# Performance work log

Hardware: AMD Instinct MI355X
Metric: run time of the kernel (lower is better)

Reference implementation:

```python
import jax, jax.numpy as jnp
import numpy as np

# ---- static ragged-batch / paging layout (known at trace time) ----
B = 4
Q_LENS = np.array([256, 512, 128, 384])        # new tokens per sequence
HIST = np.array([1792, 1024, 1536, 768])       # cached history per sequence
KV_LENS = Q_LENS + HIST
BS = 64                                        # paged-cache block size
NUM_BLOCKS = 128
H, D = 32, 128
HID = H * D
TOTAL_Q = int(Q_LENS.sum())                    # 1280 packed tokens
MAX_Q = int(Q_LENS.max())
MAX_KV = int(KV_LENS.max())
NBLK = (KV_LENS + BS - 1) // BS
MAX_BLOCKS = int(NBLK.max())                   # 32
ROPE_BASE = 10000.0

Q_START = np.concatenate([[0], np.cumsum(Q_LENS)[:-1]])
TOK_SEQ = np.repeat(np.arange(B), Q_LENS)                      # [TOTAL_Q]
TOK_LOCAL = np.concatenate([np.arange(l) for l in Q_LENS])     # [TOTAL_Q]
TOK_POS = (HIST[TOK_SEQ] + TOK_LOCAL).astype(np.int32)         # absolute positions

_perm = np.random.RandomState(0).permutation(NUM_BLOCKS)
BLOCK_TABLE = np.zeros((B, MAX_BLOCKS), np.int32)
_o = 0
for _i in range(B):
    BLOCK_TABLE[_i, :NBLK[_i]] = _perm[_o:_o + NBLK[_i]]
    _o += NBLK[_i]

_j = np.arange(MAX_Q)
# position of each padded query row; 0 for pad rows so the softmax row stays finite
POS_PAD = np.where(_j[None, :] < Q_LENS[:, None], HIST[:, None] + _j[None, :], 0)
KV_IDX = np.arange(MAX_KV)


def rope(x, pos):
    """HF-Llama rotary embedding on [T, heads, D] at absolute positions pos [T]."""
    half = D // 2
    inv_freq = 1.0 / (ROPE_BASE ** (jnp.arange(0, D, 2, dtype=jnp.float32) / D))
    ang = pos[:, None].astype(jnp.float32) * inv_freq[None, :]          # [T, D/2]
    cos = jnp.concatenate([jnp.cos(ang), jnp.cos(ang)], -1)[:, None, :]  # [T,1,D]
    sin = jnp.concatenate([jnp.sin(ang), jnp.sin(ang)], -1)[:, None, :]
    x1, x2 = x[..., :half], x[..., half:]
    rot = jnp.concatenate([-x2, x1], -1)                                 # rotate_half
    return x * cos + rot * sin


def setup_inputs() -> dict:
    key = jax.random.key(0)
    ks = jax.random.split(key, 7)
    s = 1.0 / np.sqrt(HID)
    return {
        'hidden_states': jax.random.normal(ks[0], (TOTAL_Q, HID), jnp.float32),
        'wq': jax.random.normal(ks[1], (HID, HID), jnp.float32) * s,
        'wk': jax.random.normal(ks[2], (HID, HID), jnp.float32) * s,
        'wv': jax.random.normal(ks[3], (HID, HID), jnp.float32) * s,
        'wo': jax.random.normal(ks[4], (HID, HID), jnp.float32) * s,
        'past_key': jax.random.normal(ks[5], (NUM_BLOCKS, BS, H, D), jnp.float32),
        'past_value': jax.random.normal(ks[6], (NUM_BLOCKS, BS, H, D), jnp.float32),
        'position_ids': jnp.asarray(TOK_POS, jnp.int32),
        'block_offsets': jnp.asarray(BLOCK_TABLE, jnp.int32),
    }


def reference(hidden_states, wq, wk, wv, wo, past_key, past_value,
              position_ids, block_offsets):
    # qkv projections (Linear without bias: x @ W.T)
    q = (hidden_states @ wq.T).reshape(TOTAL_Q, H, D)
    k = (hidden_states @ wk.T).reshape(TOTAL_Q, H, D)
    v = (hidden_states @ wv.T).reshape(TOTAL_Q, H, D)
    # inline RoPE at absolute (history + local) positions
    q = rope(q, position_ids)
    k = rope(k, position_ids)
    # fill paged KV cache via block table (context.fill_cache)
    dest = block_offsets[TOK_SEQ, position_ids // BS] * BS + position_ids % BS
    kc = past_key.reshape(NUM_BLOCKS * BS, H, D).at[dest].set(k)
    vc = past_value.reshape(NUM_BLOCKS * BS, H, D).at[dest].set(v)
    # paged gather of ragged KV per sequence: [B, MAX_KV, H, D]
    gath = block_offsets[:, KV_IDX // BS] * BS + KV_IDX[None, :] % BS
    K = kc[gath]
    V = vc[gath]
    # pad packed queries to [B, MAX_Q, H, D]
    Qp = jnp.zeros((B, MAX_Q, H, D), q.dtype).at[TOK_SEQ, TOK_LOCAL].set(q)
    scores = jnp.einsum('bqhd,bkhd->bhqk', Qp, K) / jnp.sqrt(jnp.float32(D))
    mask = KV_IDX[None, None, :] <= POS_PAD[:, :, None]   # causal + per-seq kv_len
    scores = jnp.where(mask[:, None, :, :], scores, jnp.float32(-1e30))
    attn = jax.nn.softmax(scores, axis=-1)
    out = jnp.einsum('bhqk,bkhd->bqhd', attn, V)
    # back to packed layout and output projection
    out = out[TOK_SEQ, TOK_LOCAL].reshape(TOTAL_Q, HID)
    return out @ wo.T
```

## Files before the change

### kernel.cpp

```cpp
#include <hip/hip_runtime.h>
#include <stdint.h>


typedef __attribute__((ext_vector_type(8))) short bf16x8;
typedef __attribute__((ext_vector_type(4))) float f32x4;
typedef __attribute__((ext_vector_type(4))) unsigned int u32x4;

__device__ __forceinline__ unsigned short f2bf(float f) {
  unsigned int u = __float_as_uint(f);
  u += 0x7fffu + ((u >> 16) & 1u);
  return (unsigned short)(u >> 16);
}

__global__ __launch_bounds__(256) void cvt_bf16(const float* __restrict__ src,
                                                unsigned short* __restrict__ dst, int n4) {
  int i = blockIdx.x * 256 + threadIdx.x;
  if (i >= n4) return;
  float4 v = ((const float4*)src)[i];
  ushort4 o;
  o.x = f2bf(v.x); o.y = f2bf(v.y); o.z = f2bf(v.z); o.w = f2bf(v.w);
  ((ushort4*)dst)[i] = o;
}

__device__ __forceinline__ void gload16(const void* g, void* l) {
  __builtin_amdgcn_global_load_lds(
      (const __attribute__((address_space(1))) unsigned int*)(g),
      (__attribute__((address_space(3))) unsigned int*)(l), 16, 0, 0);
}

__global__ __launch_bounds__(256, 2) void gemm_bt(const unsigned short* __restrict__ A,
                                                  const unsigned short* __restrict__ B,
                                                  float* __restrict__ C, int N, int K) {
  __shared__ unsigned short As[128 * 32] __attribute__((aligned(16)));
  __shared__ unsigned short Bs[128 * 32] __attribute__((aligned(16)));
  const int tid = threadIdx.x;
  const int lane = tid & 63;
  const int wv = tid >> 6;
  const int wr = wv >> 1, wc = wv & 1;
  const int mbase = blockIdx.y * 128, nbase = blockIdx.x * 128;
  const int r16 = lane >> 2;
  const int k8 = (lane & 3) * 8;
  const unsigned short* Ag0 = A + (mbase + wv * 32 + r16) * K + k8;
  const unsigned short* Ag1 = Ag0 + 16 * K;
  const unsigned short* Bg0 = B + (nbase + wv * 32 + r16) * K + k8;
  const unsigned short* Bg1 = Bg0 + 16 * K;
  unsigned short* Asl = As + wv * 1024 + lane * 8;
  unsigned short* Bsl = Bs + wv * 1024 + lane * 8;
  f32x4 acc[4][4];
#pragma unroll
  for (int i = 0; i < 4; ++i)
#pragma unroll
    for (int j = 0; j < 4; ++j) { acc[i][j][0]=0.f; acc[i][j][1]=0.f; acc[i][j][2]=0.f; acc[i][j][3]=0.f; }
  const int rowA = (wr * 64 + (lane & 15)) * 32 + (lane >> 4) * 8;
  const int colB = (wc * 64 + (lane & 15)) * 32 + (lane >> 4) * 8;
  for (int kt = 0; kt < K; kt += 32) {
    gload16(Ag0 + kt, Asl);
    gload16(Ag1 + kt, Asl + 512);
    gload16(Bg0 + kt, Bsl);
    gload16(Bg1 + kt, Bsl + 512);
    __syncthreads();
    bf16x8 af[4], bfr[4];
#pragma unroll
    for (int mi = 0; mi < 4; ++mi) af[mi] = *(const bf16x8*)(As + rowA + mi * 512);
#pragma unroll
    for (int ni = 0; ni < 4; ++ni) bfr[ni] = *(const bf16x8*)(Bs + colB + ni * 512);
#pragma unroll
    for (int mi = 0; mi < 4; ++mi)
#pragma unroll
      for (int ni = 0; ni < 4; ++ni)
        acc[mi][ni] = __builtin_amdgcn_mfma_f32_16x16x32_bf16(af[mi], bfr[ni], acc[mi][ni], 0, 0, 0);
    __syncthreads();
  }
  const int crow = mbase + wr * 64 + (lane >> 4) * 4;
  const int ccol = nbase + wc * 64 + (lane & 15);
#pragma unroll
  for (int mi = 0; mi < 4; ++mi)
#pragma unroll
    for (int ni = 0; ni < 4; ++ni)
#pragma unroll
      for (int r = 0; r < 4; ++r)
        C[(long)(crow + mi * 16 + r) * N + (ccol + ni * 16)] = acc[mi][ni][r];
}

__global__ __launch_bounds__(256) void rope_qk(const float* __restrict__ qkv, const int* __restrict__ pos,
                                               unsigned short* __restrict__ Qb, unsigned short* __restrict__ Kg) {
  int gw = blockIdx.x * 4 + (threadIdx.x >> 6);
  int lane = threadIdx.x & 63;
  int t = gw >> 5, h = gw & 31;
  int p = pos[t];
  int b = (t < 256) ? 0 : (t < 768) ? 1 : (t < 896) ? 2 : 3;
  float invf = exp2f(-(float)lane * 0.2076205059304601f);
  float ang = (float)p * invf;
  float sv = sinf(ang), cv = cosf(ang);
  const float* src = qkv + (long)t * 12288 + h * 128 + lane;
  float q1 = src[0], q2 = src[64];
  float k1 = src[4096], k2 = src[4096 + 64];
  const float scl = 0.08838834764831845f;
  unsigned short* qd = Qb + (long)t * 4096 + h * 128 + lane;
  qd[0]  = f2bf((q1 * cv - q2 * sv) * scl);
  qd[64] = f2bf((q2 * cv + q1 * sv) * scl);
  unsigned short* kd = Kg + ((long)(b * 32 + h) * 2048 + p) * 128 + lane;
  kd[0]  = f2bf(k1 * cv - k2 * sv);
  kd[64] = f2bf(k2 * cv + k1 * sv);
}

__global__ __launch_bounds__(256) void v_scatter(const float* __restrict__ qkv, unsigned short* __restrict__ VgT) {
  int tt = blockIdx.x, h = blockIdx.y;
  int b = (tt < 4) ? 0 : (tt < 12) ? 1 : (tt < 14) ? 2 : 3;
  int q0 = (b == 0) ? 0 : (b == 1) ? 256 : (b == 2) ? 768 : 896;
  int hist = (b == 0) ? 1792 : (b == 1) ? 1024 : (b == 2) ? 1536 : 768;
  int t0 = tt * 64;
  int jb = hist + t0 - q0;
  __shared__ unsigned short vt[64][130];
  int tid = threadIdx.x;
  int jj0 = tid >> 5, c4 = (tid & 31) * 4;
#pragma unroll
  for (int ps = 0; ps < 8; ++ps) {
    int jj = jj0 + ps * 8;
    float4 v = *(const float4*)(qkv + (long)(t0 + jj) * 12288 + 8192 + h * 128 + c4);
    ushort2 a, c;
    a.x = f2bf(v.x); a.y = f2bf(v.y); c.x = f2bf(v.z); c.y = f2bf(v.w);
    *(ushort2*)&vt[jj][c4] = a;
    *(ushort2*)&vt[jj][c4 + 2] = c;
  }
  __syncthreads();
  int d = tid >> 1, half = tid & 1;
  unsigned short* dst = VgT + ((long)(b * 32 + h) * 128 + d) * 2048 + jb + half * 32;
  int j0 = half * 32;
#pragma unroll
  for (int w = 0; w < 4; ++w) {
    uint4 u;
    u.x = vt[j0 + w * 8 + 0][d] | ((unsigned)vt[j0 + w * 8 + 1][d] << 16);
    u.y = vt[j0 + w * 8 + 2][d] | ((unsigned)vt[j0 + w * 8 + 3][d] << 16);
    u.z = vt[j0 + w * 8 + 4][d] | ((unsigned)vt[j0 + w * 8 + 5][d] << 16);
    u.w = vt[j0 + w * 8 + 6][d] | ((unsigned)vt[j0 + w * 8 + 7][d] << 16);
    ((uint4*)dst)[w] = u;
  }
}

__global__ __launch_bounds__(256) void gather_hist(const float* __restrict__ pk, const float* __restrict__ pv,
                                                   const int* __restrict__ btab,
                                                   unsigned short* __restrict__ Kg, unsigned short* __restrict__ VgT) {
  int gx = blockIdx.x, h = blockIdx.y;
  int b = (gx < 28) ? 0 : (gx < 44) ? 1 : (gx < 68) ? 2 : 3;
  int jt = gx - ((b == 0) ? 0 : (b == 1) ? 28 : (b == 2) ? 44 : 68);
  int slot0 = btab[b * 32 + jt] * 64;
  int jbase = jt * 64;
  __shared__ unsigned short vt[64][130];
  int tid = threadIdx.x;
  int jj0 = tid >> 5, c4 = (tid & 31) * 4;
#pragma unroll
  for (int ps = 0; ps < 8; ++ps) {
    int jj = jj0 + ps * 8;
    long off = ((long)(slot0 + jj) * 32 + h) * 128 + c4;
    float4 kk = *(const float4*)(pk + off);
    ushort4 ko;
    ko.x = f2bf(kk.x); ko.y = f2bf(kk.y); ko.z = f2bf(kk.z); ko.w = f2bf(kk.w);
    *(ushort4*)(Kg + ((long)(b * 32 + h) * 2048 + jbase + jj) * 128 + c4) = ko;
    float4 vv = *(const float4*)(pv + off);
    ushort2 a, c;
    a.x = f2bf(vv.x); a.y = f2bf(vv.y); c.x = f2bf(vv.z); c.y = f2bf(vv.w);
    *(ushort2*)&vt[jj][c4] = a;
    *(ushort2*)&vt[jj][c4 + 2] = c;
  }
  __syncthreads();
  int d = tid >> 1, half = tid & 1;
  unsigned short* dst = VgT + ((long)(b * 32 + h) * 128 + d) * 2048 + jbase + half * 32;
  int j0 = half * 32;
#pragma unroll
  for (int w = 0; w < 4; ++w) {
    uint4 u;
    u.x = vt[j0 + w * 8 + 0][d] | ((unsigned)vt[j0 + w * 8 + 1][d] << 16);
    u.y = vt[j0 + w * 8 + 2][d] | ((unsigned)vt[j0 + w * 8 + 3][d] << 16);
    u.z = vt[j0 + w * 8 + 4][d] | ((unsigned)vt[j0 + w * 8 + 5][d] << 16);
    u.w = vt[j0 + w * 8 + 6][d] | ((unsigned)vt[j0 + w * 8 + 7][d] << 16);
    ((uint4*)dst)[w] = u;
  }
}

__global__ __launch_bounds__(256) void attn_part(const unsigned short* __restrict__ Qb,
                                                 const unsigned short* __restrict__ Kg,
                                                 const unsigned short* __restrict__ VgT,
                                                 const int* __restrict__ pos,
                                                 float* __restrict__ Opart,
                                                 float* __restrict__ ml) {
  __shared__ char lds[32768] __attribute__((aligned(16)));
  int qt = blockIdx.x, h = blockIdx.y, ck = blockIdx.z;
  int tid = threadIdx.x;
  int wv = tid >> 6, lane = tid & 63;
  int b = (qt < 4) ? 0 : (qt < 12) ? 1 : (qt < 14) ? 2 : 3;
  int qb = qt * 64 + wv * 16;
  int qcol = lane & 15, g = lane >> 4;
  int t = qb + qcol;
  int p = pos[t];
  int pmax_wave = pos[qb + 15];
  int pmax_blk = pos[qt * 64 + 63];
  int kv_begin = ck * 512;
  if (kv_begin > pmax_blk) return;
  int kv_end = pmax_blk + 1;
  if (kv_end > kv_begin + 512) kv_end = kv_begin + 512;
  int nt = (kv_end - kv_begin + 31) >> 5;

  const char* KbhB = (const char*)(Kg + (long)(b * 32 + h) * 2048 * 128);
  const char* VbhB = (const char*)(VgT + (long)(b * 32 + h) * 128 * 2048);

  const int d0 = tid * 16, d1 = 4096 + tid * 16;
  const int ksrc0 = d0 ^ (((d0 >> 8) & 7) << 4);
  const int ksrc1 = d1 ^ (((d1 >> 8) & 7) << 4);
  const int vrow0 = d0 >> 6, vrow1 = d1 >> 6;
  const int vsrc0 = vrow0 * 4096 + ((d0 & 63) ^ ((vrow0 & 3) << 4));
  const int vsrc1 = vrow1 * 4096 + ((d1 & 63) ^ ((vrow1 & 3) << 4));

#define STAGE(kv0, buf)                                                     \
  {                                                                          \
    const char* Ksrc = KbhB + (long)(kv0) * 256;                             \
    const char* Vsrc = VbhB + (long)(kv0) * 2;                               \
    char* Kd = lds + (buf) * 8192;                                           \
    char* Vd = lds + 16384 + (buf) * 8192;                                   \
    gload16(Ksrc + ksrc0, Kd + d0);                                          \
    gload16(Ksrc + ksrc1, Kd + d1);                                          \
    gload16(Vsrc + vsrc0, Vd + d0);                                          \
    gload16(Vsrc + vsrc1, Vd + d1);                                          \
  }

  const unsigned short* Qp = Qb + (long)t * 4096 + h * 128 + g * 8;
  bf16x8 qf[4];
#pragma unroll
  for (int c = 0; c < 4; ++c) qf[c] = *(const bf16x8*)(Qp + c * 32);

  const int kswz = ((qcol & 7) << 4);
  const int vswz = (g * 16) ^ ((qcol & 3) << 4);

  float m = -1e30f, lsum = 0.f;
  f32x4 o[8];
#pragma unroll
  for (int i = 0; i < 8; ++i) { o[i][0]=0.f; o[i][1]=0.f; o[i][2]=0.f; o[i][3]=0.f; }

  STAGE(kv_begin, 0);

  for (int it = 0; it < nt; ++it) {
    int cur = it & 1;
    int kv0 = kv_begin + it * 32;
    if (it + 1 < nt) {
      STAGE(kv0 + 32, cur ^ 1);
      asm volatile("s_waitcnt vmcnt(4)" ::: "memory");
    } else {
      asm volatile("s_waitcnt vmcnt(0)" ::: "memory");
    }
    __builtin_amdgcn_sched_barrier(0);
    __builtin_amdgcn_s_barrier();
    if (kv0 <= pmax_wave) {
      const char* Kc = lds + cur * 8192;
      const char* Vc = lds + 16384 + cur * 8192;
      f32x4 s0, s1;
      s0[0]=0.f;s0[1]=0.f;s0[2]=0.f;s0[3]=0.f;
      s1[0]=0.f;s1[1]=0.f;s1[2]=0.f;s1[3]=0.f;
#pragma unroll
      for (int c = 0; c < 4; ++c) {
        int colb = (g * 16 + c * 64) ^ kswz;
        bf16x8 k0 = *(const bf16x8*)(Kc + qcol * 256 + colb);
        bf16x8 k1 = *(const bf16x8*)(Kc + 4096 + qcol * 256 + colb);
        s0 = __builtin_amdgcn_mfma_f32_16x16x32_bf16(k0, qf[c], s0, 0, 0, 0);
        s1 = __builtin_amdgcn_mfma_f32_16x16x32_bf16(k1, qf[c], s1, 0, 0, 0);
      }
      int kvg = kv0 + g * 4;
      float sv[8];
#pragma unroll
      for (int r = 0; r < 4; ++r) {
        sv[r]     = (kvg + r      <= p) ? s0[r] : -1e30f;
        sv[r + 4] = (kvg + 16 + r <= p) ? s1[r] : -1e30f;
      }
      float mt = sv[0];
#pragma unroll
      for (int i = 1; i < 8; ++i) mt = fmaxf(mt, sv[i]);
      mt = fmaxf(mt, __shfl_xor(mt, 16));
      mt = fmaxf(mt, __shfl_xor(mt, 32));
      float mnew = fmaxf(m, mt);
      float corr = __expf(m - mnew);
      float ssum = 0.f;
      float pvv[8];
#pragma unroll
      for (int i = 0; i < 8; ++i) { pvv[i] = __expf(sv[i] - mnew); ssum += pvv[i]; }
      ssum += __shfl_xor(ssum, 16);
      ssum += __shfl_xor(ssum, 32);
      lsum = lsum * corr + ssum;
      m = mnew;
#pragma unroll
      for (int df = 0; df < 8; ++df) o[df] *= corr;
      unsigned pk0 = (unsigned)f2bf(pvv[0]) | ((unsigned)f2bf(pvv[1]) << 16);
      unsigned pk1 = (unsigned)f2bf(pvv[2]) | ((unsigned)f2bf(pvv[3]) << 16);
      unsigned pk2 = (unsigned)f2bf(pvv[4]) | ((unsigned)f2bf(pvv[5]) << 16);
      unsigned pk3 = (unsigned)f2bf(pvv[6]) | ((unsigned)f2bf(pvv[7]) << 16);
      int s0l = ((g & 1) * 32) + qcol;
      int s1l = s0l + 16;
      unsigned a0 = (unsigned)__shfl((int)pk0, s0l), a1 = (unsigned)__shfl((int)pk1, s0l);
      unsigned a2 = (unsigned)__shfl((int)pk2, s0l), a3 = (unsigned)__shfl((int)pk3, s0l);
      unsigned b0 = (unsigned)__shfl((int)pk0, s1l), b1 = (unsigned)__shfl((int)pk1, s1l);
      unsigned b2 = (unsigned)__shfl((int)pk2, s1l), b3 = (unsigned)__shfl((int)pk3, s1l);
      bool hi = (g >= 2);
      u32x4 wv4;
      wv4[0] = hi ? a2 : a0; wv4[1] = hi ? a3 : a1;
      wv4[2] = hi ? b2 : b0; wv4[3] = hi ? b3 : b1;
      bf16x8 pfrag = __builtin_bit_cast(bf16x8, wv4);
#pragma unroll
      for (int df = 0; df < 8; ++df) {
        bf16x8 vf = *(const bf16x8*)(Vc + (df * 16 + qcol) * 64 + vswz);
        o[df] = __builtin_amdgcn_mfma_f32_16x16x32_bf16(vf, pfrag, o[df], 0, 0, 0);
      }
    }
    __builtin_amdgcn_s_barrier();
  }
#undef STAGE
  long pbase = (long)((qt * 32 + h) * 4 + ck);
  float* Op = Opart + pbase * 8192 + (wv * 16 + qcol) * 128 + g * 4;
#pragma unroll
  for (int df = 0; df < 8; ++df)
#pragma unroll
    for (int r = 0; r < 4; ++r)
      Op[df * 16 + r] = o[df][r];
  if (g == 0) {
    float* mlp = ml + pbase * 128 + (wv * 16 + qcol) * 2;
    mlp[0] = m;
    mlp[1] = lsum;
  }
}

__global__ __launch_bounds__(256) void attn_comb(const float* __restrict__ Opart,
                                                 const float* __restrict__ ml,
                                                 const int* __restrict__ pos,
                                                 unsigned short* __restrict__ Ao) {
  int qt = blockIdx.x, h = blockIdx.y;
  int tid = threadIdx.x;
  int q = tid >> 2, dq = (tid & 3) * 32;
  int t = qt * 64 + q;
  int p = pos[t];
  int ncv = (p >> 9) + 1;
  if (ncv > 4) ncv = 4;
  long base = (long)(qt * 32 + h) * 4;
  float M = -1e30f;
#pragma unroll
  for (int c = 0; c < 4; ++c)
    if (c < ncv) M = fmaxf(M, ml[(base + c) * 128 + q * 2]);
  float L = 0.f;
#pragma unroll
  for (int c = 0; c < 4; ++c)
    if (c < ncv) L += __expf(ml[(base + c) * 128 + q * 2] - M) * ml[(base + c) * 128 + q * 2 + 1];
  f32x4 acc[8];
#pragma unroll
  for (int i = 0; i < 8; ++i) { acc[i][0]=0.f; acc[i][1]=0.f; acc[i][2]=0.f; acc[i][3]=0.f; }
#pragma unroll
  for (int c = 0; c < 4; ++c)
    if (c < ncv) {
      float wc = __expf(ml[(base + c) * 128 + q * 2] - M);
      const f32x4* src = (const f32x4*)(Opart + (base + c) * 8192 + q * 128 + dq);
#pragma unroll
      for (int i = 0; i < 8; ++i) {
        f32x4 s = src[i];
        acc[i][0] += wc * s[0]; acc[i][1] += wc * s[1];
        acc[i][2] += wc * s[2]; acc[i][3] += wc * s[3];
      }
    }
  float inv = 1.f / L;
  unsigned short* dst = Ao + (long)t * 4096 + h * 128 + dq;
#pragma unroll
  for (int i = 0; i < 8; ++i) {
    ushort4 ov;
    ov.x = f2bf(acc[i][0] * inv); ov.y = f2bf(acc[i][1] * inv);
    ov.z = f2bf(acc[i][2] * inv); ov.w = f2bf(acc[i][3] * inv);
    *(ushort4*)(dst + i * 4) = ov;
  }
}

extern "C" void kernel_launch(void* const* d_in, const int* in_sizes, int n_in,
                              void* d_out, int out_size, void* d_ws, size_t ws_size,
                              hipStream_t stream) {
  const float* hs   = (const float*)d_in[0];
  const float* wq   = (const float*)d_in[1];
  const float* wk   = (const float*)d_in[2];
  const float* wvp  = (const float*)d_in[3];
  const float* wo   = (const float*)d_in[4];
  const float* pkey = (const float*)d_in[5];
  const float* pval = (const float*)d_in[6];
  const int* pos    = (const int*)d_in[7];
  const int* btab   = (const int*)d_in[8];

  unsigned short* Wqkv = (unsigned short*)d_ws;
  unsigned short* Wo   = Wqkv + (size_t)12288 * 4096;
  unsigned short* Hb   = Wo + (size_t)4096 * 4096;
  float* qkv           = (float*)(Hb + (size_t)1280 * 4096);
  unsigned short* Qbf  = (unsigned short*)(qkv + (size_t)1280 * 12288);
  unsigned short* Kg   = Qbf + (size_t)1280 * 4096;
  unsigned short* VgT  = Kg + (size_t)4 * 32 * 2048 * 128;
  unsigned short* Aob  = VgT + (size_t)4 * 32 * 2048 * 128;
  float* Opart = (float*)d_ws;
  float* mlb   = (float*)((char*)d_ws + 83886080);
  if (ws_size < 362807296ull) return;

  cvt_bf16<<<16384, 256, 0, stream>>>(wq,  Wqkv,                 4194304);
  cvt_bf16<<<16384, 256, 0, stream>>>(wk,  Wqkv + 16777216,      4194304);
  cvt_bf16<<<16384, 256, 0, stream>>>(wvp, Wqkv + 33554432,      4194304);
  cvt_bf16<<<16384, 256, 0, stream>>>(wo,  Wo,                   4194304);
  cvt_bf16<<<5120,  256, 0, stream>>>(hs,  Hb,                   1310720);

  gemm_bt<<<dim3(96, 10), 256, 0, stream>>>(Hb, Wqkv, qkv, 12288, 4096);
  rope_qk<<<10240, 256, 0, stream>>>(qkv, pos, Qbf, Kg);
  v_scatter<<<dim3(20, 32), 256, 0, stream>>>(qkv, VgT);
  gather_hist<<<dim3(80, 32), 256, 0, stream>>>(pkey, pval, btab, Kg, VgT);
  attn_part<<<dim3(20, 32, 4), 256, 0, stream>>>(Qbf, Kg, VgT, pos, Opart, mlb);
  attn_comb<<<dim3(20, 32), 256, 0, stream>>>(Opart, mlb, pos, Aob);
  gemm_bt<<<dim3(32, 10), 256, 0, stream>>>(Aob, Wo, (float*)d_out, 4096, 4096);
}
```

Measured before the change: 514.3 us.

## Add 256x256-tile bf16 MFMA GEMM for the fused QKV projection

Adds a new GEMM kernel for the QKV projection. It uses 512 threads, 256x256 output tiles and 128 KB of double-buffered dynamic LDS loaded via global_load_lds, with an XOR swizzle to reduce LDS bank conflicts. MFMA groups are interleaved with fragment loads and raised with s_setprio. The larger tile is meant to raise arithmetic intensity and cut repeated global/L2 traffic for A and B compared with the 128x128 kernel. The trade-off: the grid drops to 240 blocks (under one per CU), and 128 KB of LDS per block prevents two blocks per CU. It also relies on large dynamic LDS being accepted at launch.

```diff
diff --git a/kernel.cpp b/kernel.cpp
--- a/kernel.cpp
+++ b/kernel.cpp
@@ -26,6 +26,151 @@
   __builtin_amdgcn_global_load_lds(
       (const __attribute__((address_space(1))) unsigned int*)(g),
       (__attribute__((address_space(3))) unsigned int*)(l), 16, 0, 0);
+}
+
+__global__ __launch_bounds__(512, 2) void gemm256(const unsigned short* __restrict__ A,
+                                                  const unsigned short* __restrict__ B,
+                                                  float* __restrict__ C, int N, int K) {
+  extern __shared__ char lds[];
+  const int tid = threadIdx.x;
+  const int lane = tid & 63;
+  const int wid = tid >> 6;
+  const int wm = wid >> 2, wn = wid & 3;
+  const int qcol = lane & 15, g = lane >> 4;
+  const int mbase = blockIdx.y * 256, nbase = blockIdx.x * 256;
+  const long Kb = (long)K * 2;
+
+  const int srow = tid >> 3;
+  const int scb = ((tid & 7) * 16) ^ (((srow >> 2) & 3) << 5);
+  const char* Ab = (const char*)A;
+  const char* Bb = (const char*)B;
+  const long asrc0 = (long)(mbase + srow) * Kb + scb;
+  const long asrc1 = (long)(mbase + 64 + srow) * Kb + scb;
+  const long asrc2 = (long)(mbase + 128 + srow) * Kb + scb;
+  const long asrc3 = (long)(mbase + 192 + srow) * Kb + scb;
+  const long bsrc0 = (long)(nbase + srow) * Kb + scb;
+  const long bsrc1 = (long)(nbase + 64 + srow) * Kb + scb;
+  const long bsrc2 = (long)(nbase + 128 + srow) * Kb + scb;
+  const long bsrc3 = (long)(nbase + 192 + srow) * Kb + scb;
+  const int dst0 = tid * 16;
+
+#define STAGE256(kt, bs) {                                                   \
+    long ko = (long)(kt) * 128;                                              \
+    char* Lw = lds + (bs) * 32768;                                           \
+    gload16(Ab + asrc0 + ko, Lw + dst0);                                     \
+    gload16(Ab + asrc1 + ko, Lw + 8192 + dst0);                              \
+    gload16(Ab + asrc2 + ko, Lw + 16384 + dst0);                             \
+    gload16(Ab + asrc3 + ko, Lw + 24576 + dst0);                             \
+    gload16(Bb + bsrc0 + ko, Lw + 65536 + dst0);                             \
+    gload16(Bb + bsrc1 + ko, Lw + 65536 + 8192 + dst0);                      \
+    gload16(Bb + bsrc2 + ko, Lw + 65536 + 16384 + dst0);                     \
+    gload16(Bb + bsrc3 + ko, Lw + 65536 + 24576 + dst0);                     \
+  }
+
+  const int swl = ((qcol >> 2) & 3) << 5;
+  const int c0 = (g * 16) ^ swl;
+  const int c1 = (64 + g * 16) ^ swl;
+  const int aoff = (wm * 128 + qcol) * 128;
+  const int boff = 65536 + (wn * 64 + qcol) * 128;
+
+  f32x4 acc[8][4];
+#pragma unroll
+  for (int i = 0; i < 8; ++i)
+#pragma unroll
+    for (int j = 0; j < 4; ++j) { acc[i][j][0]=0.f; acc[i][j][1]=0.f; acc[i][j][2]=0.f; acc[i][j][3]=0.f; }
+
+  STAGE256(0, 0);
+  const int nkt = K >> 6;
+#pragma unroll 1
+  for (int kt = 0; kt < nkt; ++kt) {
+    const int cur = kt & 1;
+    const char* Lc = lds + cur * 32768;
+    if (kt + 1 < nkt) {
+      STAGE256(kt + 1, cur ^ 1);
+      asm volatile("s_waitcnt vmcnt(8)" ::: "memory");
+    } else {
+      asm volatile("s_waitcnt vmcnt(0)" ::: "memory");
+    }
+    __builtin_amdgcn_sched_barrier(0);
+    __builtin_amdgcn_s_barrier();
+    __builtin_amdgcn_sched_barrier(0);
+
+    bf16x8 af[4][2], bfr[4][2];
+#pragma unroll
+    for (int mi = 0; mi < 4; ++mi) {
+      af[mi][0] = *(const bf16x8*)(Lc + aoff + mi * 2048 + c0);
+      af[mi][1] = *(const bf16x8*)(Lc + aoff + mi * 2048 + c1);
+    }
+#pragma unroll
+    for (int ni = 0; ni < 2; ++ni) {
+      bfr[ni][0] = *(const bf16x8*)(Lc + boff + ni * 2048 + c0);
+      bfr[ni][1] = *(const bf16x8*)(Lc + boff + ni * 2048 + c1);
+    }
+    asm volatile("s_waitcnt lgkmcnt(0)" ::: "memory");
+    __builtin_amdgcn_sched_barrier(0);
+    __builtin_amdgcn_s_setprio(1);
+#pragma unroll
+    for (int mi = 0; mi < 4; ++mi)
+#pragma unroll
+      for (int ni = 0; ni < 2; ++ni) {
+        acc[mi][ni] = __builtin_amdgcn_mfma_f32_16x16x32_bf16(af[mi][0], bfr[ni][0], acc[mi][ni], 0, 0, 0);
+        acc[mi][ni] = __builtin_amdgcn_mfma_f32_16x16x32_bf16(af[mi][1], bfr[ni][1], acc[mi][ni], 0, 0, 0);
+      }
+    __builtin_amdgcn_s_setprio(0);
+#pragma unroll
+    for (int ni = 2; ni < 4; ++ni) {
+      bfr[ni][0] = *(const bf16x8*)(Lc + boff + ni * 2048 + c0);
+      bfr[ni][1] = *(const bf16x8*)(Lc + boff + ni * 2048 + c1);
+    }
+    asm volatile("s_waitcnt lgkmcnt(0)" ::: "memory");
+    __builtin_amdgcn_sched_barrier(0);
+    __builtin_amdgcn_s_setprio(1);
+#pragma unroll
+    for (int mi = 0; mi < 4; ++mi)
+#pragma unroll
+      for (int ni = 2; ni < 4; ++ni) {
+        acc[mi][ni] = __builtin_amdgcn_mfma_f32_16x16x32_bf16(af[mi][0], bfr[ni][0], acc[mi][ni], 0, 0, 0);
+        acc[mi][ni] = __builtin_amdgcn_mfma_f32_16x16x32_bf16(af[mi][1], bfr[ni][1], acc[mi][ni], 0, 0, 0);
+      }
+    __builtin_amdgcn_s_setprio(0);
+#pragma unroll
+    for (int mi = 0; mi < 4; ++mi) {
+      af[mi][0] = *(const bf16x8*)(Lc + aoff + (mi + 4) * 2048 + c0);
+      af[mi][1] = *(const bf16x8*)(Lc + aoff + (mi + 4) * 2048 + c1);
+    }
+    asm volatile("s_waitcnt lgkmcnt(0)" ::: "memory");
+    __builtin_amdgcn_sched_barrier(0);
+    __builtin_amdgcn_s_setprio(1);
+#pragma unroll
+    for (int mi = 0; mi < 4; ++mi)
+#pragma unroll
+      for (int ni = 2; ni < 4; ++ni) {
+        acc[mi + 4][ni] = __builtin_amdgcn_mfma_f32_16x16x32_bf16(af[mi][0], bfr[ni][0], acc[mi + 4][ni], 0, 0, 0);
+        acc[mi + 4][ni] = __builtin_amdgcn_mfma_f32_16x16x32_bf16(af[mi][1], bfr[ni][1], acc[mi + 4][ni], 0, 0, 0);
+      }
+    __builtin_amdgcn_s_setprio(0);
+    __builtin_amdgcn_s_setprio(1);
+#pragma unroll
+    for (int mi = 0; mi < 4; ++mi)
+#pragma unroll
+      for (int ni = 0; ni < 2; ++ni) {
+        acc[mi + 4][ni] = __builtin_amdgcn_mfma_f32_16x16x32_bf16(af[mi][0], bfr[ni][0], acc[mi + 4][ni], 0, 0, 0);
+        acc[mi + 4][ni] = __builtin_amdgcn_mfma_f32_16x16x32_bf16(af[mi][1], bfr[ni][1], acc[mi + 4][ni], 0, 0, 0);
+      }
+    __builtin_amdgcn_s_setprio(0);
+    __builtin_amdgcn_s_barrier();
+    __builtin_amdgcn_sched_barrier(0);
+  }
+#undef STAGE256
+  const int crow = mbase + wm * 128 + g * 4;
+  const int ccol = nbase + wn * 64 + qcol;
+#pragma unroll
+  for (int mi = 0; mi < 8; ++mi)
+#pragma unroll
+    for (int ni = 0; ni < 4; ++ni)
+#pragma unroll
+      for (int r = 0; r < 4; ++r)
+        C[(long)(crow + mi * 16 + r) * N + (ccol + ni * 16)] = acc[mi][ni][r];
 }
 
 __global__ __launch_bounds__(256, 2) void gemm_bt(const unsigned short* __restrict__ A,
@@ -402,7 +547,7 @@
   cvt_bf16<<<16384, 256, 0, stream>>>(wo,  Wo,                   4194304);
   cvt_bf16<<<5120,  256, 0, stream>>>(hs,  Hb,                   1310720);
 
-  gemm_bt<<<dim3(96, 10), 256, 0, stream>>>(Hb, Wqkv, qkv, 12288, 4096);
+  gemm256<<<dim3(48, 5), 512, 131072, stream>>>(Hb, Wqkv, qkv, 12288, 4096);
   rope_qk<<<10240, 256, 0, stream>>>(qkv, pos, Qbf, Kg);
   v_scatter<<<dim3(20, 32), 256, 0, stream>>>(qkv, VgT);
   gather_hist<<<dim3(80, 32), 256, 0, stream>>>(pkey, pval, btab, Kg, VgT);
```

Result: faster. 495.4 us (-3.7%).

## Use 256x256-tile multistage LDS GEMM for the fused QKV projection

Applied to the files above, without the earlier changes.

Adds a new bf16 MFMA GEMM kernel with 256x256 output tiles, 512 threads and a 4-slot LDS ring buffer. It prefetches two k-steps ahead with direct global-to-LDS loads and explicit vmcnt waits, and the QKV projection now runs on it instead of the 128x128 gemm_bt. The larger tile is meant to raise operand reuse and cut global and L2 traffic per FLOP. In exchange it uses 128KB of dynamic LDS, which allows only one block per CU, and launches just 240 blocks. Its LDS reads are also unswizzled, so bank conflicts are possible.

```diff
diff --git a/kernel.cpp b/kernel.cpp
--- a/kernel.cpp
+++ b/kernel.cpp
@@ -26,6 +26,87 @@
   __builtin_amdgcn_global_load_lds(
       (const __attribute__((address_space(1))) unsigned int*)(g),
       (__attribute__((address_space(3))) unsigned int*)(l), 16, 0, 0);
+}
+
+__global__ __launch_bounds__(512, 2) void gemm256(const unsigned short* __restrict__ A,
+                                                  const unsigned short* __restrict__ B,
+                                                  float* __restrict__ C, int N, int K) {
+  extern __shared__ char lds[];
+  const int tid = threadIdx.x;
+  const int lane = tid & 63;
+  const int wid = tid >> 6;
+  const int wm = wid >> 2, wn = wid & 3;
+  const int qcol = lane & 15, g = lane >> 4;
+  const int mbase = blockIdx.y * 256, nbase = blockIdx.x * 256;
+  const long Kb = (long)K * 2;
+
+  const char* Ab = (const char*)A;
+  const char* Bb = (const char*)B;
+  const long asrc0 = (long)(mbase + (tid >> 2)) * Kb + (tid & 3) * 16;
+  const long asrc1 = asrc0 + 128 * Kb;
+  const long bsrc0 = (long)(nbase + (tid >> 2)) * Kb + (tid & 3) * 16;
+  const long bsrc1 = bsrc0 + 128 * Kb;
+  const int dst0 = tid * 16;
+
+#define STG(kt, bs) {                                                        \
+    long ko = (long)(kt) * 64;                                               \
+    char* L = lds + (bs) * 32768;                                            \
+    gload16(Ab + asrc0 + ko, L + dst0);                                      \
+    gload16(Ab + asrc1 + ko, L + 8192 + dst0);                               \
+    gload16(Bb + bsrc0 + ko, L + 16384 + dst0);                              \
+    gload16(Bb + bsrc1 + ko, L + 24576 + dst0);                              \
+  }
+
+  const int aoff = (wm * 128 + qcol) * 64 + g * 16;
+  const int boff = 16384 + (wn * 64 + qcol) * 64 + g * 16;
+
+  f32x4 acc[8][4];
+#pragma unroll
+  for (int i = 0; i < 8; ++i)
+#pragma unroll
+    for (int j = 0; j < 4; ++j) { acc[i][j][0]=0.f; acc[i][j][1]=0.f; acc[i][j][2]=0.f; acc[i][j][3]=0.f; }
+
+  const int nkt = K >> 5;
+  STG(0, 0);
+  STG(1, 1);
+#pragma unroll 1
+  for (int kt = 0; kt < nkt; ++kt) {
+    if (kt + 2 < nkt) {
+      STG(kt + 2, (kt + 2) & 3);
+      asm volatile("s_waitcnt vmcnt(8)" ::: "memory");
+    } else if (kt + 1 < nkt) {
+      asm volatile("s_waitcnt vmcnt(4)" ::: "memory");
+    } else {
+      asm volatile("s_waitcnt vmcnt(0)" ::: "memory");
+    }
+    __builtin_amdgcn_sched_barrier(0);
+    __builtin_amdgcn_s_barrier();
+    __builtin_amdgcn_sched_barrier(0);
+
+    const char* Lc = lds + (kt & 3) * 32768;
+    bf16x8 af[8], bfv[4];
+#pragma unroll
+    for (int mi = 0; mi < 8; ++mi) af[mi] = *(const bf16x8*)(Lc + aoff + mi * 1024);
+#pragma unroll
+    for (int ni = 0; ni < 4; ++ni) bfv[ni] = *(const bf16x8*)(Lc + boff + ni * 1024);
+    __builtin_amdgcn_s_setprio(1);
+#pragma unroll
+    for (int mi = 0; mi < 8; ++mi)
+#pragma unroll
+      for (int ni = 0; ni < 4; ++ni)
+        acc[mi][ni] = __builtin_amdgcn_mfma_f32_16x16x32_bf16(af[mi], bfv[ni], acc[mi][ni], 0, 0, 0);
+    __builtin_amdgcn_s_setprio(0);
+  }
+#undef STG
+  const int crow = mbase + wm * 128 + g * 4;
+  const int ccol = nbase + wn * 64 + qcol;
+#pragma unroll
+  for (int mi = 0; mi < 8; ++mi)
+#pragma unroll
+    for (int ni = 0; ni < 4; ++ni)
+#pragma unroll
+      for (int r = 0; r < 4; ++r)
+        C[(long)(crow + mi * 16 + r) * N + (ccol + ni * 16)] = acc[mi][ni][r];
 }
 
 __global__ __launch_bounds__(256, 2) void gemm_bt(const unsigned short* __restrict__ A,
@@ -402,7 +483,7 @@
   cvt_bf16<<<16384, 256, 0, stream>>>(wo,  Wo,                   4194304);
   cvt_bf16<<<5120,  256, 0, stream>>>(hs,  Hb,                   1310720);
 
-  gemm_bt<<<dim3(96, 10), 256, 0, stream>>>(Hb, Wqkv, qkv, 12288, 4096);
+  gemm256<<<dim3(48, 5), 512, 131072, stream>>>(Hb, Wqkv, qkv, 12288, 4096);
   rope_qk<<<10240, 256, 0, stream>>>(qkv, pos, Qbf, Kg);
   v_scatter<<<dim3(20, 32), 256, 0, stream>>>(qkv, VgT);
   gather_hist<<<dim3(80, 32), 256, 0, stream>>>(pkey, pval, btab, Kg, VgT);
```

Measured after the change: 486.6 us. 5.4% less time.
